# Kernel tuning notes

Measured on AMD Instinct MI355X. Metric: run time of the kernel, lower is better.

Reference implementation:

```python
import jax, jax.numpy as jnp
import numpy as np

N_NODES = 50000
N_EDGES = 1600000
N_GRAPHS = 64


def gcn_conv(x, edge_index, W, b):
    """GCNConv: out = D^{-1/2} (A + I) D^{-1/2} X W + b (symmetric norm, self-loops)."""
    n = x.shape[0]
    src = jnp.concatenate([edge_index[0], jnp.arange(n)])  # add self-loops
    dst = jnp.concatenate([edge_index[1], jnp.arange(n)])
    deg = jax.ops.segment_sum(jnp.ones_like(dst, dtype=x.dtype), dst, num_segments=n)
    dinv = jax.lax.rsqrt(jnp.maximum(deg, 1.0))
    norm = dinv[src] * dinv[dst]                      # [E+N]
    h = x @ W                                          # transform first (smaller gather)
    msg = norm[:, None] * h[src]                       # [E+N, out_dim]
    out = jax.ops.segment_sum(msg, dst, num_segments=n)
    return out + b


def global_mean_pool(x, batch, num_graphs):
    s = jax.ops.segment_sum(x, batch, num_segments=num_graphs)
    cnt = jax.ops.segment_sum(jnp.ones((x.shape[0],), x.dtype), batch, num_segments=num_graphs)
    return s / jnp.maximum(cnt, 1.0)[:, None]


def setup_inputs() -> dict:
    key = jax.random.key(0)
    ks = jax.random.split(key, 6)
    x = jax.random.normal(ks[0], (N_NODES, 256), dtype=jnp.float32)
    edge_index = jax.random.randint(ks[1], (2, N_EDGES), 0, N_NODES, dtype=jnp.int64)
    batch = jnp.sort(jax.random.randint(ks[2], (N_NODES,), 0, N_GRAPHS, dtype=jnp.int64))
    W1 = jax.random.normal(ks[3], (256, 256), dtype=jnp.float32) * (1.0 / np.sqrt(256))
    b1 = jnp.zeros((256,), jnp.float32)
    W2 = jax.random.normal(ks[4], (256, 10), dtype=jnp.float32) * (1.0 / np.sqrt(256))
    b2 = jnp.zeros((10,), jnp.float32)
    return {"x": x, "edge_index": edge_index, "batch": batch,
            "W1": W1, "b1": b1, "W2": W2, "b2": b2}


def reference(x, edge_index, batch, W1, b1, W2, b2):
    h = gcn_conv(x, edge_index, W1, b1)
    h = jax.nn.elu(h)
    # dropout: identity (inference mode, training=False)
    h = gcn_conv(h, edge_index, W2, b2)
    h = jax.nn.elu(h)
    g = global_mean_pool(h, batch, N_GRAPHS)          # [num_graphs, num_class]
    return jax.nn.log_softmax(g, axis=-1)
```

## Files before the change

### kernel.cpp

```cpp
#include <hip/hip_runtime.h>
#include <hip/hip_bf16.h>
#include <math.h>

typedef unsigned int uint;
typedef unsigned short ushort;
typedef unsigned char uchar;

typedef __attribute__((ext_vector_type(8))) short bf16x8;
typedef __attribute__((ext_vector_type(4))) float f32x4;
typedef __attribute__((ext_vector_type(2))) float f32x2;

#define SBLK_SHIFT 12
#define SBLK_STRIDE 16
#define H2S 16

__device__ __forceinline__ ushort f2bf(float f) {
    uint u = __float_as_uint(f);
    uint rounding = 0x7fffu + ((u >> 16) & 1u);
    return (ushort)((u + rounding) >> 16);
}
__device__ __forceinline__ float elu(float x) {
    return x > 0.f ? x : expm1f(x);
}

__global__ void count2_kernel(const int* __restrict__ src, const int* __restrict__ dst, int E,
                              int* __restrict__ cnt2) {
    int i = blockIdx.x * blockDim.x + threadIdx.x;
    int stride = gridDim.x * blockDim.x;
    for (; i < E; i += stride)
        atomicAdd(&cnt2[dst[i] * SBLK_STRIDE + (src[i] >> SBLK_SHIFT)], 1);
}

__global__ void scan1_kernel(const int* __restrict__ cnt, int M, int* __restrict__ partials) {
    __shared__ int sh[256];
    int i = blockIdx.x * 256 + threadIdx.x;
    sh[threadIdx.x] = (i < M) ? cnt[i] : 0;
    __syncthreads();
    for (int s = 128; s > 0; s >>= 1) {
        if (threadIdx.x < s) sh[threadIdx.x] += sh[threadIdx.x + s];
        __syncthreads();
    }
    if (threadIdx.x == 0) partials[blockIdx.x] = sh[0];
}

__global__ __launch_bounds__(256) void scan2_kernel(const int* __restrict__ partials, int nb,
                                                    int* __restrict__ pscan) {
    __shared__ int tsum[256];
    int t = threadIdx.x;
    int pref[16];
    int s = 0;
    #pragma unroll
    for (int j = 0; j < 16; ++j) {
        int idx = t * 16 + j;
        int v = (idx < nb) ? partials[idx] : 0;
        pref[j] = s;
        s += v;
    }
    tsum[t] = s;
    __syncthreads();
    for (int d = 1; d < 256; d <<= 1) {
        int x = (t >= d) ? tsum[t - d] : 0;
        __syncthreads();
        tsum[t] += x;
        __syncthreads();
    }
    int base = (t == 0) ? 0 : tsum[t - 1];
    #pragma unroll
    for (int j = 0; j < 16; ++j) {
        int idx = t * 16 + j;
        if (idx < nb) pscan[idx] = base + pref[j];
    }
}

__global__ void scan3_kernel(const int* __restrict__ cnt, int M, const int* __restrict__ pscan,
                             int* __restrict__ offs2, int* __restrict__ cursor2) {
    __shared__ int sh[256];
    int t = threadIdx.x;
    int i = blockIdx.x * 256 + t;
    int v = (i < M) ? cnt[i] : 0;
    sh[t] = v;
    __syncthreads();
    for (int d = 1; d < 256; d <<= 1) {
        int x = (t >= d) ? sh[t - d] : 0;
        __syncthreads();
        sh[t] += x;
        __syncthreads();
    }
    int excl = sh[t] - v;
    int base = pscan[blockIdx.x];
    if (i < M) {
        offs2[i]   = base + excl;
        cursor2[i] = base + excl;
    }
}

__global__ void post_kernel(const int* __restrict__ offs2, int NN, int E,
                            int* __restrict__ offs, float* __restrict__ dinv) {
    int n = blockIdx.x * blockDim.x + threadIdx.x;
    if (n >= NN) return;
    int o = offs2[n * SBLK_STRIDE];
    int nxt = (n == NN - 1) ? E : offs2[(n + 1) * SBLK_STRIDE];
    offs[n] = o;
    dinv[n] = rsqrtf((float)(nxt - o) + 1.0f);
    if (n == NN - 1) offs[NN] = E;
}

__global__ __launch_bounds__(256) void scatter_kernel(const int* __restrict__ src,
                                                      const int* __restrict__ dst, int E,
                                                      int* __restrict__ cursor2,
                                                      int* __restrict__ ssrc, int NN) {
    int grp = blockIdx.x & 7;
    int per = (NN + 7) >> 3;
    int lo = grp * per;
    int hi = min(NN, lo + per);
    int bid = blockIdx.x >> 3;
    int nb  = gridDim.x >> 3;
    int i = bid * blockDim.x + threadIdx.x;
    int stride = nb * blockDim.x;
    for (; i < E; i += stride) {
        int d = dst[i];
        if (d >= lo && d < hi) {
            int s = src[i];
            int pos = atomicAdd(&cursor2[d * SBLK_STRIDE + (s >> SBLK_SHIFT)], 1);
            ssrc[pos] = s;
        }
    }
}

__global__ void gstart_kernel(const int* __restrict__ batch, int NN, int NG,
                              int* __restrict__ gstart) {
    int g = blockIdx.x * blockDim.x + threadIdx.x;
    if (g > NG) return;
    int lo = 0, hi = NN;
    while (lo < hi) {
        int mid = (lo + hi) >> 1;
        if (batch[mid] < g) lo = mid + 1; else hi = mid;
    }
    gstart[g] = lo;
}

__global__ __launch_bounds__(256) void wtrans_kernel(const float* __restrict__ W,
                                                     ushort* __restrict__ WT) {
    __shared__ float T[64][68];
    int b = blockIdx.x;
    int kt = (b >> 2) * 64, nt = (b & 3) * 64;
    int t = threadIdx.x;
    int r = t >> 4, c4 = (t & 15) * 4;
    #pragma unroll
    for (int h = 0; h < 4; ++h) {
        int rr = r + h * 16;
        float4 v = *reinterpret_cast<const float4*>(&W[(size_t)(kt + rr) * 256 + nt + c4]);
        *reinterpret_cast<float4*>(&T[rr][c4]) = v;
    }
    __syncthreads();
    int nr = t >> 2, ks = (t & 3) * 16;
    uint o[8];
    #pragma unroll
    for (int i = 0; i < 16; i += 2) {
        float f0 = T[ks + i][nr];
        float f1 = T[ks + i + 1][nr];
        o[i >> 1] = (uint)f2bf(f0) | ((uint)f2bf(f1) << 16);
    }
    size_t base = (size_t)(nt + nr) * 256 + kt + ks;
    *reinterpret_cast<uint4*>(&WT[base])     = make_uint4(o[0], o[1], o[2], o[3]);
    *reinterpret_cast<uint4*>(&WT[base + 8]) = make_uint4(o[4], o[5], o[6], o[7]);
}

#define G1_STRIDE 40
__global__ __launch_bounds__(256) void gemm1_mfma_kernel(const float* __restrict__ X,
                                                         const ushort* __restrict__ W1T,
                                                         const float* __restrict__ dinv,
                                                         uchar* __restrict__ H1, int M) {
    __shared__ ushort Xs[64 * G1_STRIDE];
    __shared__ ushort Ws[256 * G1_STRIDE];
    __shared__ float  Dvs[64];
    int t = threadIdx.x;
    int row0 = blockIdx.x * 64;
    int lane = t & 63;
    int w = t >> 6;
    int lr = lane & 15;
    int lg = lane >> 4;

    if (t < 64) {
        int grow = row0 + t;
        Dvs[t] = (grow < M) ? dinv[grow] : 0.f;
    }

    f32x4 acc[4][4];
    #pragma unroll
    for (int j = 0; j < 4; ++j)
        #pragma unroll
        for (int i = 0; i < 4; ++i)
            acc[j][i] = (f32x4){0.f, 0.f, 0.f, 0.f};

    for (int k0 = 0; k0 < 256; k0 += 32) {
        #pragma unroll
        for (int h = 0; h < 2; ++h) {
            int u = t + h * 256;
            int row = u >> 3;
            int kq = (u & 7) * 4;
            int grow = row0 + row;
            float4 v = make_float4(0.f, 0.f, 0.f, 0.f);
            if (grow < M) v = *reinterpret_cast<const float4*>(&X[(size_t)grow * 256 + k0 + kq]);
            uint lo = (uint)f2bf(v.x) | ((uint)f2bf(v.y) << 16);
            uint hi = (uint)f2bf(v.z) | ((uint)f2bf(v.w) << 16);
            *reinterpret_cast<uint2*>(&Xs[row * G1_STRIDE + kq]) = make_uint2(lo, hi);
        }
        #pragma unroll
        for (int h = 0; h < 4; ++h) {
            int u = t + h * 256;
            int n = u >> 2;
            int seg = u & 3;
            uint4 wv = *reinterpret_cast<const uint4*>(&W1T[(size_t)n * 256 + k0 + seg * 8]);
            *reinterpret_cast<uint4*>(&Ws[n * G1_STRIDE + seg * 8]) = wv;
        }
        __syncthreads();
        bf16x8 wf[4], xf[4];
        #pragma unroll
        for (int j = 0; j < 4; ++j)
            wf[j] = *reinterpret_cast<const bf16x8*>(&Ws[(w * 64 + j * 16 + lr) * G1_STRIDE + lg * 8]);
        #pragma unroll
        for (int i = 0; i < 4; ++i)
            xf[i] = *reinterpret_cast<const bf16x8*>(&Xs[(i * 16 + lr) * G1_STRIDE + lg * 8]);
        #pragma unroll
        for (int j = 0; j < 4; ++j)
            #pragma unroll
            for (int i = 0; i < 4; ++i)
                acc[j][i] = __builtin_amdgcn_mfma_f32_16x16x32_bf16(wf[j], xf[i], acc[j][i], 0, 0, 0);
        __syncthreads();
    }

    #pragma unroll
    for (int mi = 0; mi < 4; ++mi) {
        int grow = row0 + mi * 16 + lr;
        float dv = Dvs[mi * 16 + lr];
        bool ok = grow < M;
        #pragma unroll
        for (int nj = 0; nj < 4; ++nj) {
            f32x4 a = acc[nj][mi];
            int pk = __builtin_amdgcn_cvt_pk_fp8_f32(a[0] * dv, a[1] * dv, 0, false);
            pk     = __builtin_amdgcn_cvt_pk_fp8_f32(a[2] * dv, a[3] * dv, pk, true);
            if (ok) {
                int col = w * 64 + nj * 16 + lg * 4;
                *reinterpret_cast<uint*>(&H1[(size_t)grow * 256 + col]) = (uint)pk;
            }
        }
    }
}

__global__ __launch_bounds__(256) void agg1_gemm2_kernel(
    const uchar* __restrict__ H1, const int* __restrict__ offs, const int* __restrict__ ssrc,
    const float* __restrict__ dinv, const float* __restrict__ b1, const float* __restrict__ W2,
    float* __restrict__ H2, int NN) {
    int lane = threadIdx.x & 63;
    int node = blockIdx.x * 4 + (threadIdx.x >> 6);
    if (node >= NN) return;
    int beg = offs[node], end = offs[node + 1];
    int col = lane * 4;
    const uchar* H1c = H1 + col;
    float acc0 = 0.f, acc1 = 0.f, acc2 = 0.f, acc3 = 0.f;
    int i = beg;
    for (; i + 3 < end; i += 4) {
        int s0 = ssrc[i], s1 = ssrc[i + 1], s2 = ssrc[i + 2], s3 = ssrc[i + 3];
        uint p0 = *reinterpret_cast<const uint*>(H1c + (size_t)s0 * 256);
        uint p1 = *reinterpret_cast<const uint*>(H1c + (size_t)s1 * 256);
        uint p2 = *reinterpret_cast<const uint*>(H1c + (size_t)s2 * 256);
        uint p3 = *reinterpret_cast<const uint*>(H1c + (size_t)s3 * 256);
        f32x2 l0 = __builtin_amdgcn_cvt_pk_f32_fp8((int)p0, false);
        f32x2 h0 = __builtin_amdgcn_cvt_pk_f32_fp8((int)p0, true);
        f32x2 l1 = __builtin_amdgcn_cvt_pk_f32_fp8((int)p1, false);
        f32x2 h1 = __builtin_amdgcn_cvt_pk_f32_fp8((int)p1, true);
        f32x2 l2 = __builtin_amdgcn_cvt_pk_f32_fp8((int)p2, false);
        f32x2 h2 = __builtin_amdgcn_cvt_pk_f32_fp8((int)p2, true);
        f32x2 l3 = __builtin_amdgcn_cvt_pk_f32_fp8((int)p3, false);
        f32x2 h3 = __builtin_amdgcn_cvt_pk_f32_fp8((int)p3, true);
        acc0 += (l0.x + l1.x) + (l2.x + l3.x);
        acc1 += (l0.y + l1.y) + (l2.y + l3.y);
        acc2 += (h0.x + h1.x) + (h2.x + h3.x);
        acc3 += (h0.y + h1.y) + (h2.y + h3.y);
    }
    for (; i < end; ++i) {
        int s = ssrc[i];
        uint p = *reinterpret_cast<const uint*>(H1c + (size_t)s * 256);
        f32x2 l = __builtin_amdgcn_cvt_pk_f32_fp8((int)p, false);
        f32x2 h = __builtin_amdgcn_cvt_pk_f32_fp8((int)p, true);
        acc0 += l.x; acc1 += l.y; acc2 += h.x; acc3 += h.y;
    }
    {
        uint p = *reinterpret_cast<const uint*>(H1c + (size_t)node * 256);
        f32x2 l = __builtin_amdgcn_cvt_pk_f32_fp8((int)p, false);
        f32x2 h = __builtin_amdgcn_cvt_pk_f32_fp8((int)p, true);
        acc0 += l.x; acc1 += l.y; acc2 += h.x; acc3 += h.y;
    }
    float dn = dinv[node];
    float a0 = elu(fmaf(acc0, dn, b1[col + 0]));
    float a1 = elu(fmaf(acc1, dn, b1[col + 1]));
    float a2 = elu(fmaf(acc2, dn, b1[col + 2]));
    float a3 = elu(fmaf(acc3, dn, b1[col + 3]));
    float hv = 0.f;
    #pragma unroll
    for (int c = 0; c < 10; ++c) {
        float p = a0 * W2[(col + 0) * 10 + c]
                + a1 * W2[(col + 1) * 10 + c]
                + a2 * W2[(col + 2) * 10 + c]
                + a3 * W2[(col + 3) * 10 + c];
        #pragma unroll
        for (int m = 1; m < 64; m <<= 1) p += __shfl_xor(p, m, 64);
        if (lane == c) hv = p;
    }
    if (lane < 10) H2[(size_t)node * H2S + lane] = dn * hv;
}

__global__ __launch_bounds__(256) void agg2_elu_kernel(
    const float* __restrict__ H2, const int* __restrict__ offs, const int* __restrict__ ssrc,
    const float* __restrict__ dinv, const float* __restrict__ b2,
    float* __restrict__ H2act, int NN) {
    int t = threadIdx.x;
    int node = blockIdx.x * 8 + (t >> 5);
    if (node >= NN) return;
    int sub = t & 31;
    int c = sub & 15;
    int e2 = sub >> 4;
    int beg = offs[node], end = offs[node + 1];
    float acc = 0.f;
    int i = beg + e2;
    for (; i + 6 < end; i += 8) {
        int s0 = ssrc[i], s1 = ssrc[i + 2], s2 = ssrc[i + 4], s3 = ssrc[i + 6];
        float h0 = H2[(size_t)s0 * H2S + c];
        float h1 = H2[(size_t)s1 * H2S + c];
        float h2 = H2[(size_t)s2 * H2S + c];
        float h3 = H2[(size_t)s3 * H2S + c];
        acc += (h0 + h1) + (h2 + h3);
    }
    for (; i < end; i += 2) acc += H2[(size_t)ssrc[i] * H2S + c];
    if (e2 == 0) acc += H2[(size_t)node * H2S + c];
    acc += __shfl_xor(acc, 16, 64);
    if (sub < 10) {
        float dn = dinv[node];
        H2act[(size_t)node * 10 + c] = elu(fmaf(dn, acc, b2[c]));
    }
}

__global__ __launch_bounds__(320) void pool_final_kernel(
    const float* __restrict__ H2act, const int* __restrict__ gstart,
    float* __restrict__ out, int NG) {
    __shared__ float red[32][10];
    __shared__ float m[10];
    __shared__ float s_lse;
    int g = blockIdx.x;
    int t = threadIdx.x;
    int grp = t / 10;
    int c = t - grp * 10;
    int lo = gstart[g], hi = gstart[g + 1];
    float acc = 0.f;
    if (grp < 32) {
        for (int n = lo + grp; n < hi; n += 32) acc += H2act[(size_t)n * 10 + c];
        red[grp][c] = acc;
    }
    __syncthreads();
    if (t < 10) {
        float s = 0.f;
        #pragma unroll
        for (int j = 0; j < 32; ++j) s += red[j][t];
        m[t] = s / fmaxf((float)(hi - lo), 1.0f);
    }
    __syncthreads();
    if (t == 0) {
        float mx = -1e30f;
        for (int c2 = 0; c2 < 10; ++c2) mx = fmaxf(mx, m[c2]);
        float s = 0.f;
        for (int c2 = 0; c2 < 10; ++c2) s += expf(m[c2] - mx);
        s_lse = logf(s) + mx;
    }
    __syncthreads();
    if (t < 10) out[g * 10 + t] = m[t] - s_lse;
}

extern "C" void kernel_launch(void* const* d_in, const int* in_sizes, int n_in,
                              void* d_out, int out_size, void* d_ws, size_t ws_size,
                              hipStream_t stream) {
    const float* x     = (const float*)d_in[0];
    const int*   eidx  = (const int*)d_in[1];
    const int*   batch = (const int*)d_in[2];
    const float* W1    = (const float*)d_in[3];
    const float* b1    = (const float*)d_in[4];
    const float* W2    = (const float*)d_in[5];
    const float* b2    = (const float*)d_in[6];

    int NN = in_sizes[0] / 256;
    int E  = in_sizes[1] / 2;
    int NG = out_size / 10;
    const int* src = eidx;
    const int* dst = eidx + E;

    int M2 = NN * SBLK_STRIDE;

    char* ws = (char*)d_ws;
    size_t off = 0;
    auto alloc = [&](size_t bytes) -> void* {
        void* p = ws + off;
        off += (bytes + 255) & ~((size_t)255);
        return p;
    };
    int*    cnt2     = (int*)alloc((size_t)M2 * 4);
    int*    offs2    = (int*)alloc((size_t)M2 * 4);
    int*    cursor2  = (int*)alloc((size_t)M2 * 4);
    int*    offs     = (int*)alloc((size_t)(NN + 1) * 4);
    int*    partials = (int*)alloc(4096 * 4);
    int*    pscan    = (int*)alloc(4096 * 4);
    float*  dinv     = (float*)alloc((size_t)NN * 4);
    int*    gstart   = (int*)alloc((size_t)(NG + 1) * 4);
    ushort* W1T      = (ushort*)alloc((size_t)256 * 256 * 2);
    int*    ssrc     = (int*)alloc((size_t)E * 4);
    uchar*  H1       = (uchar*)alloc((size_t)NN * 256);
    float*  H2       = (float*)alloc((size_t)NN * H2S * 4);
    float*  H2act    = (float*)alloc((size_t)NN * 10 * 4);

    hipMemsetAsync(cnt2, 0, (size_t)M2 * 4, stream);

    int nb2 = (M2 + 255) / 256;
    count2_kernel <<<1024, 256, 0, stream>>>(src, dst, E, cnt2);
    scan1_kernel  <<<nb2, 256, 0, stream>>>(cnt2, M2, partials);
    scan2_kernel  <<<1, 256, 0, stream>>>(partials, nb2, pscan);
    scan3_kernel  <<<nb2, 256, 0, stream>>>(cnt2, M2, pscan, offs2, cursor2);
    post_kernel   <<<(NN + 255) / 256, 256, 0, stream>>>(offs2, NN, E, offs, dinv);
    scatter_kernel<<<2048, 256, 0, stream>>>(src, dst, E, cursor2, ssrc, NN);
    gstart_kernel <<<1, 128, 0, stream>>>(batch, NN, NG, gstart);
    wtrans_kernel <<<16, 256, 0, stream>>>(W1, W1T);
    gemm1_mfma_kernel<<<(NN + 63) / 64, 256, 0, stream>>>(x, W1T, dinv, H1, NN);
    agg1_gemm2_kernel<<<(NN + 3) / 4, 256, 0, stream>>>(H1, offs, ssrc, dinv, b1, W2, H2, NN);
    agg2_elu_kernel  <<<(NN + 7) / 8, 256, 0, stream>>>(H2, offs, ssrc, dinv, b2, H2act, NN);
    pool_final_kernel<<<NG, 320, 0, stream>>>(H2act, gstart, (float*)d_out, NG);
}
```

Before: 308.7 us.

## Drop source-bucketed CSR, fuse degree into scan, split wave across edges in agg1

```diff
diff --git a/kernel.cpp b/kernel.cpp
--- a/kernel.cpp
+++ b/kernel.cpp
@@ -10,8 +10,6 @@
 typedef __attribute__((ext_vector_type(4))) float f32x4;
 typedef __attribute__((ext_vector_type(2))) float f32x2;
 
-#define SBLK_SHIFT 12
-#define SBLK_STRIDE 16
 #define H2S 16
 
 __device__ __forceinline__ ushort f2bf(float f) {
@@ -23,12 +21,10 @@
     return x > 0.f ? x : expm1f(x);
 }
 
-__global__ void count2_kernel(const int* __restrict__ src, const int* __restrict__ dst, int E,
-                              int* __restrict__ cnt2) {
+__global__ void count_kernel(const int* __restrict__ dst, int E, int* __restrict__ cnt) {
     int i = blockIdx.x * blockDim.x + threadIdx.x;
     int stride = gridDim.x * blockDim.x;
-    for (; i < E; i += stride)
-        atomicAdd(&cnt2[dst[i] * SBLK_STRIDE + (src[i] >> SBLK_SHIFT)], 1);
+    for (; i < E; i += stride) atomicAdd(&cnt[dst[i]], 1);
 }
 
 __global__ void scan1_kernel(const int* __restrict__ cnt, int M, int* __restrict__ partials) {
@@ -73,7 +69,8 @@
 }
 
 __global__ void scan3_kernel(const int* __restrict__ cnt, int M, const int* __restrict__ pscan,
-                             int* __restrict__ offs2, int* __restrict__ cursor2) {
+                             int* __restrict__ offs, int* __restrict__ cursor,
+                             float* __restrict__ dinv) {
     __shared__ int sh[256];
     int t = threadIdx.x;
     int i = blockIdx.x * 256 + t;
@@ -86,28 +83,20 @@
         sh[t] += x;
         __syncthreads();
     }
-    int excl = sh[t] - v;
+    int incl = sh[t];
+    int excl = incl - v;
     int base = pscan[blockIdx.x];
     if (i < M) {
-        offs2[i]   = base + excl;
-        cursor2[i] = base + excl;
-    }
-}
-
-__global__ void post_kernel(const int* __restrict__ offs2, int NN, int E,
-                            int* __restrict__ offs, float* __restrict__ dinv) {
-    int n = blockIdx.x * blockDim.x + threadIdx.x;
-    if (n >= NN) return;
-    int o = offs2[n * SBLK_STRIDE];
-    int nxt = (n == NN - 1) ? E : offs2[(n + 1) * SBLK_STRIDE];
-    offs[n] = o;
-    dinv[n] = rsqrtf((float)(nxt - o) + 1.0f);
-    if (n == NN - 1) offs[NN] = E;
+        offs[i]   = base + excl;
+        cursor[i] = base + excl;
+        dinv[i]   = rsqrtf((float)v + 1.0f);
+        if (i == M - 1) offs[M] = base + incl;
+    }
 }
 
 __global__ __launch_bounds__(256) void scatter_kernel(const int* __restrict__ src,
                                                       const int* __restrict__ dst, int E,
-                                                      int* __restrict__ cursor2,
+                                                      int* __restrict__ cursor,
                                                       int* __restrict__ ssrc, int NN) {
     int grp = blockIdx.x & 7;
     int per = (NN + 7) >> 3;
@@ -120,23 +109,10 @@
     for (; i < E; i += stride) {
         int d = dst[i];
         if (d >= lo && d < hi) {
-            int s = src[i];
-            int pos = atomicAdd(&cursor2[d * SBLK_STRIDE + (s >> SBLK_SHIFT)], 1);
-            ssrc[pos] = s;
+            int pos = atomicAdd(&cursor[d], 1);
+            ssrc[pos] = src[i];
         }
     }
-}
-
-__global__ void gstart_kernel(const int* __restrict__ batch, int NN, int NG,
-                              int* __restrict__ gstart) {
-    int g = blockIdx.x * blockDim.x + threadIdx.x;
-    if (g > NG) return;
-    int lo = 0, hi = NN;
-    while (lo < hi) {
-        int mid = (lo + hi) >> 1;
-        if (batch[mid] < g) lo = mid + 1; else hi = mid;
-    }
-    gstart[g] = lo;
 }
 
 __global__ __launch_bounds__(256) void wtrans_kernel(const float* __restrict__ W,
@@ -255,57 +231,76 @@
     int lane = threadIdx.x & 63;
     int node = blockIdx.x * 4 + (threadIdx.x >> 6);
     if (node >= NN) return;
+    int half = lane >> 5;
+    int fl = lane & 31;
+    const uchar* H1c = H1 + fl * 8;
     int beg = offs[node], end = offs[node + 1];
-    int col = lane * 4;
-    const uchar* H1c = H1 + col;
-    float acc0 = 0.f, acc1 = 0.f, acc2 = 0.f, acc3 = 0.f;
-    int i = beg;
-    for (; i + 3 < end; i += 4) {
-        int s0 = ssrc[i], s1 = ssrc[i + 1], s2 = ssrc[i + 2], s3 = ssrc[i + 3];
-        uint p0 = *reinterpret_cast<const uint*>(H1c + (size_t)s0 * 256);
-        uint p1 = *reinterpret_cast<const uint*>(H1c + (size_t)s1 * 256);
-        uint p2 = *reinterpret_cast<const uint*>(H1c + (size_t)s2 * 256);
-        uint p3 = *reinterpret_cast<const uint*>(H1c + (size_t)s3 * 256);
-        f32x2 l0 = __builtin_amdgcn_cvt_pk_f32_fp8((int)p0, false);
-        f32x2 h0 = __builtin_amdgcn_cvt_pk_f32_fp8((int)p0, true);
-        f32x2 l1 = __builtin_amdgcn_cvt_pk_f32_fp8((int)p1, false);
-        f32x2 h1 = __builtin_amdgcn_cvt_pk_f32_fp8((int)p1, true);
-        f32x2 l2 = __builtin_amdgcn_cvt_pk_f32_fp8((int)p2, false);
-        f32x2 h2 = __builtin_amdgcn_cvt_pk_f32_fp8((int)p2, true);
-        f32x2 l3 = __builtin_amdgcn_cvt_pk_f32_fp8((int)p3, false);
-        f32x2 h3 = __builtin_amdgcn_cvt_pk_f32_fp8((int)p3, true);
-        acc0 += (l0.x + l1.x) + (l2.x + l3.x);
-        acc1 += (l0.y + l1.y) + (l2.y + l3.y);
-        acc2 += (h0.x + h1.x) + (h2.x + h3.x);
-        acc3 += (h0.y + h1.y) + (h2.y + h3.y);
-    }
-    for (; i < end; ++i) {
+    float a0 = 0.f, a1 = 0.f, a2 = 0.f, a3 = 0.f, a4 = 0.f, a5 = 0.f, a6 = 0.f, a7 = 0.f;
+
+    int i = beg + half;
+    for (; i + 6 < end; i += 8) {
+        int s0 = ssrc[i], s1 = ssrc[i + 2], s2 = ssrc[i + 4], s3 = ssrc[i + 6];
+        uint2 p0 = *reinterpret_cast<const uint2*>(H1c + (size_t)s0 * 256);
+        uint2 p1 = *reinterpret_cast<const uint2*>(H1c + (size_t)s1 * 256);
+        uint2 p2 = *reinterpret_cast<const uint2*>(H1c + (size_t)s2 * 256);
+        uint2 p3 = *reinterpret_cast<const uint2*>(H1c + (size_t)s3 * 256);
+        #pragma unroll
+        for (int q = 0; q < 4; ++q) {
+            uint2 p = (q == 0) ? p0 : (q == 1) ? p1 : (q == 2) ? p2 : p3;
+            f32x2 l = __builtin_amdgcn_cvt_pk_f32_fp8((int)p.x, false);
+            f32x2 m = __builtin_amdgcn_cvt_pk_f32_fp8((int)p.x, true);
+            f32x2 n = __builtin_amdgcn_cvt_pk_f32_fp8((int)p.y, false);
+            f32x2 o = __builtin_amdgcn_cvt_pk_f32_fp8((int)p.y, true);
+            a0 += l.x; a1 += l.y; a2 += m.x; a3 += m.y;
+            a4 += n.x; a5 += n.y; a6 += o.x; a7 += o.y;
+        }
+    }
+    for (; i < end; i += 2) {
         int s = ssrc[i];
-        uint p = *reinterpret_cast<const uint*>(H1c + (size_t)s * 256);
-        f32x2 l = __builtin_amdgcn_cvt_pk_f32_fp8((int)p, false);
-        f32x2 h = __builtin_amdgcn_cvt_pk_f32_fp8((int)p, true);
-        acc0 += l.x; acc1 += l.y; acc2 += h.x; acc3 += h.y;
-    }
-    {
-        uint p = *reinterpret_cast<const uint*>(H1c + (size_t)node * 256);
-        f32x2 l = __builtin_amdgcn_cvt_pk_f32_fp8((int)p, false);
-        f32x2 h = __builtin_amdgcn_cvt_pk_f32_fp8((int)p, true);
-        acc0 += l.x; acc1 += l.y; acc2 += h.x; acc3 += h.y;
-    }
+        uint2 p = *reinterpret_cast<const uint2*>(H1c + (size_t)s * 256);
+        f32x2 l = __builtin_amdgcn_cvt_pk_f32_fp8((int)p.x, false);
+        f32x2 m = __builtin_amdgcn_cvt_pk_f32_fp8((int)p.x, true);
+        f32x2 n = __builtin_amdgcn_cvt_pk_f32_fp8((int)p.y, false);
+        f32x2 o = __builtin_amdgcn_cvt_pk_f32_fp8((int)p.y, true);
+        a0 += l.x; a1 += l.y; a2 += m.x; a3 += m.y;
+        a4 += n.x; a5 += n.y; a6 += o.x; a7 += o.y;
+    }
+    if (half == 0) {
+        uint2 p = *reinterpret_cast<const uint2*>(H1c + (size_t)node * 256);
+        f32x2 l = __builtin_amdgcn_cvt_pk_f32_fp8((int)p.x, false);
+        f32x2 m = __builtin_amdgcn_cvt_pk_f32_fp8((int)p.x, true);
+        f32x2 n = __builtin_amdgcn_cvt_pk_f32_fp8((int)p.y, false);
+        f32x2 o = __builtin_amdgcn_cvt_pk_f32_fp8((int)p.y, true);
+        a0 += l.x; a1 += l.y; a2 += m.x; a3 += m.y;
+        a4 += n.x; a5 += n.y; a6 += o.x; a7 += o.y;
+    }
+    a0 += __shfl_xor(a0, 32, 64);
+    a1 += __shfl_xor(a1, 32, 64);
+    a2 += __shfl_xor(a2, 32, 64);
+    a3 += __shfl_xor(a3, 32, 64);
+    a4 += __shfl_xor(a4, 32, 64);
+    a5 += __shfl_xor(a5, 32, 64);
+    a6 += __shfl_xor(a6, 32, 64);
+    a7 += __shfl_xor(a7, 32, 64);
+
     float dn = dinv[node];
-    float a0 = elu(fmaf(acc0, dn, b1[col + 0]));
-    float a1 = elu(fmaf(acc1, dn, b1[col + 1]));
-    float a2 = elu(fmaf(acc2, dn, b1[col + 2]));
-    float a3 = elu(fmaf(acc3, dn, b1[col + 3]));
+    int c0 = fl * 8;
+    float e0 = elu(fmaf(a0, dn, b1[c0 + 0]));
+    float e1 = elu(fmaf(a1, dn, b1[c0 + 1]));
+    float e2 = elu(fmaf(a2, dn, b1[c0 + 2]));
+    float e3 = elu(fmaf(a3, dn, b1[c0 + 3]));
+    float e4 = elu(fmaf(a4, dn, b1[c0 + 4]));
+    float e5 = elu(fmaf(a5, dn, b1[c0 + 5]));
+    float e6 = elu(fmaf(a6, dn, b1[c0 + 6]));
+    float e7 = elu(fmaf(a7, dn, b1[c0 + 7]));
     float hv = 0.f;
     #pragma unroll
     for (int c = 0; c < 10; ++c) {
-        float p = a0 * W2[(col + 0) * 10 + c]
-                + a1 * W2[(col + 1) * 10 + c]
-                + a2 * W2[(col + 2) * 10 + c]
-                + a3 * W2[(col + 3) * 10 + c];
-        #pragma unroll
-        for (int m = 1; m < 64; m <<= 1) p += __shfl_xor(p, m, 64);
+        const float* W2c = W2 + (size_t)c0 * 10 + c;
+        float p = e0 * W2c[0]  + e1 * W2c[10] + e2 * W2c[20] + e3 * W2c[30]
+                + e4 * W2c[40] + e5 * W2c[50] + e6 * W2c[60] + e7 * W2c[70];
+        #pragma unroll
+        for (int m = 1; m < 32; m <<= 1) p += __shfl_xor(p, m, 64);
         if (lane == c) hv = p;
     }
     if (lane < 10) H2[(size_t)node * H2S + lane] = dn * hv;
@@ -342,19 +337,22 @@
 }
 
 __global__ __launch_bounds__(320) void pool_final_kernel(
-    const float* __restrict__ H2act, const int* __restrict__ gstart,
+    const float* __restrict__ H2act, const int* __restrict__ batch, int NN,
     float* __restrict__ out, int NG) {
     __shared__ float red[32][10];
     __shared__ float m[10];
     __shared__ float s_lse;
     int g = blockIdx.x;
     int t = threadIdx.x;
+    int lo = 0, hi = NN;
+    while (lo < hi) { int mid = (lo + hi) >> 1; if (batch[mid] < g) lo = mid + 1; else hi = mid; }
+    int lo2 = lo, hi2 = NN;
+    while (lo2 < hi2) { int mid = (lo2 + hi2) >> 1; if (batch[mid] < g + 1) lo2 = mid + 1; else hi2 = mid; }
     int grp = t / 10;
     int c = t - grp * 10;
-    int lo = gstart[g], hi = gstart[g + 1];
     float acc = 0.f;
     if (grp < 32) {
-        for (int n = lo + grp; n < hi; n += 32) acc += H2act[(size_t)n * 10 + c];
+        for (int n = lo + grp; n < lo2; n += 32) acc += H2act[(size_t)n * 10 + c];
         red[grp][c] = acc;
     }
     __syncthreads();
@@ -362,7 +360,7 @@
         float s = 0.f;
         #pragma unroll
         for (int j = 0; j < 32; ++j) s += red[j][t];
-        m[t] = s / fmaxf((float)(hi - lo), 1.0f);
+        m[t] = s / fmaxf((float)(lo2 - lo), 1.0f);
     }
     __syncthreads();
     if (t == 0) {
@@ -393,8 +391,6 @@
     const int* src = eidx;
     const int* dst = eidx + E;
 
-    int M2 = NN * SBLK_STRIDE;
-
     char* ws = (char*)d_ws;
     size_t off = 0;
     auto alloc = [&](size_t bytes) -> void* {
@@ -402,33 +398,29 @@
         off += (bytes + 255) & ~((size_t)255);
         return p;
     };
-    int*    cnt2     = (int*)alloc((size_t)M2 * 4);
-    int*    offs2    = (int*)alloc((size_t)M2 * 4);
-    int*    cursor2  = (int*)alloc((size_t)M2 * 4);
+    int*    cnt      = (int*)alloc((size_t)NN * 4);
     int*    offs     = (int*)alloc((size_t)(NN + 1) * 4);
+    int*    cursor   = (int*)alloc((size_t)NN * 4);
     int*    partials = (int*)alloc(4096 * 4);
     int*    pscan    = (int*)alloc(4096 * 4);
     float*  dinv     = (float*)alloc((size_t)NN * 4);
-    int*    gstart   = (int*)alloc((size_t)(NG + 1) * 4);
     ushort* W1T      = (ushort*)alloc((size_t)256 * 256 * 2);
     int*    ssrc     = (int*)alloc((size_t)E * 4);
     uchar*  H1       = (uchar*)alloc((size_t)NN * 256);
     float*  H2       = (float*)alloc((size_t)NN * H2S * 4);
     float*  H2act    = (float*)alloc((size_t)NN * 10 * 4);
 
-    hipMemsetAsync(cnt2, 0, (size_t)M2 * 4, stream);
-
-    int nb2 = (M2 + 255) / 256;
-    count2_kernel <<<1024, 256, 0, stream>>>(src, dst, E, cnt2);
-    scan1_kernel  <<<nb2, 256, 0, stream>>>(cnt2, M2, partials);
-    scan2_kernel  <<<1, 256, 0, stream>>>(partials, nb2, pscan);
-    scan3_kernel  <<<nb2, 256, 0, stream>>>(cnt2, M2, pscan, offs2, cursor2);
-    post_kernel   <<<(NN + 255) / 256, 256, 0, stream>>>(offs2, NN, E, offs, dinv);
-    scatter_kernel<<<2048, 256, 0, stream>>>(src, dst, E, cursor2, ssrc, NN);
-    gstart_kernel <<<1, 128, 0, stream>>>(batch, NN, NG, gstart);
+    hipMemsetAsync(cnt, 0, (size_t)NN * 4, stream);
+
+    int nb = (NN + 255) / 256;
+    count_kernel  <<<1024, 256, 0, stream>>>(dst, E, cnt);
+    scan1_kernel  <<<nb, 256, 0, stream>>>(cnt, NN, partials);
+    scan2_kernel  <<<1, 256, 0, stream>>>(partials, nb, pscan);
+    scan3_kernel  <<<nb, 256, 0, stream>>>(cnt, NN, pscan, offs, cursor, dinv);
+    scatter_kernel<<<2048, 256, 0, stream>>>(src, dst, E, cursor, ssrc, NN);
     wtrans_kernel <<<16, 256, 0, stream>>>(W1, W1T);
     gemm1_mfma_kernel<<<(NN + 63) / 64, 256, 0, stream>>>(x, W1T, dinv, H1, NN);
     agg1_gemm2_kernel<<<(NN + 3) / 4, 256, 0, stream>>>(H1, offs, ssrc, dinv, b1, W2, H2, NN);
     agg2_elu_kernel  <<<(NN + 7) / 8, 256, 0, stream>>>(H2, offs, ssrc, dinv, b2, H2act, NN);
-    pool_final_kernel<<<NG, 320, 0, stream>>>(H2act, gstart, (float*)d_out, NG);
-}
+    pool_final_kernel<<<NG, 320, 0, stream>>>(H2act, batch, NN, (float*)d_out, NG);
+}
```

Result: slower. 364.2 us (+18.0%).
